# Optimization experiments

Hardware: AMD Instinct MI355X
Metric: run time of the kernel (lower is better)

## Reference

```python
import jax, jax.numpy as jnp
import numpy as np

B, CIN, X, Y = 4, 3, 128, 128
D, L, DEPTH, OUT = 64, 8, 4, 1
GRID_RANGE = 1.0
LN_EPS = 1e-5
YR = Y // 2 + 1


def _build_phi_f():
    # 1D Hilbert-matrix eigenbases along each axis, outer product, then rfft2.
    def top_eigvecs(n):
        i = np.arange(n)
        Z = 1.0 / (i[:, None] + i[None, :] + 1.0)  # Hilbert matrix, float64
        w, V = np.linalg.eigh(Z)
        idx = np.argsort(-w)[:L]
        return V.T[idx]  # (L, n)

    Vx = top_eigvecs(X)
    Vy = top_eigvecs(Y)
    phi = Vx[:, :, None] * Vy[:, None, :]  # (L, X, Y) separable eigenfunctions
    Phi_f = np.fft.rfft2(phi, s=(X, Y))  # (L, X, YR)
    return jnp.asarray(Phi_f, dtype=jnp.complex64)


def setup_inputs() -> dict:
    key = jax.random.key(0)
    ks = jax.random.split(key, 16)
    u = lambda k, shape, bound: jax.random.uniform(k, shape, jnp.float32, -bound, bound)
    inv = 1.0 / np.sqrt(D)
    inp = {
        "x": jax.random.normal(ks[0], (B, CIN, X, Y), jnp.float32),
        "Phi_f": _build_phi_f(),  # constant buffer
        "lift_w": u(ks[1], (D, CIN + 2), 1.0 / np.sqrt(CIN + 2)),
        "lift_b": u(ks[2], (D,), 1.0 / np.sqrt(CIN + 2)),
        "Theta": u(ks[3], (DEPTH, L, D, D), 1.0 / D),  # kaiming_uniform(a=sqrt(5)) ~ U(-1/d, 1/d)
        "glu_val_w": u(ks[4], (DEPTH, D, D), inv),
        "glu_val_b": u(ks[5], (DEPTH, D), inv),
        "glu_gate_w": u(ks[6], (DEPTH, D, D), inv),
        "glu_gate_b": u(ks[7], (DEPTH, D), inv),
        "ln_g": jnp.ones((DEPTH, D), jnp.float32),
        "ln_b": jnp.zeros((DEPTH, D), jnp.float32),
        "head_w": u(ks[8], (OUT, D), inv),
        "head_b": u(ks[9], (OUT,), inv),
    }
    return inp


def _stu_layer(h, Phi_f, Theta, vw, vb, gw, gb, g, b):
    # LayerNorm over channel dim (torch LayerNorm on channels-last view)
    ht = jnp.transpose(h, (0, 2, 3, 1))  # (B, X, Y, D)
    mu = jnp.mean(ht, axis=-1, keepdims=True)
    var = jnp.var(ht, axis=-1, keepdims=True)
    zt = (ht - mu) * jax.lax.rsqrt(var + LN_EPS) * g + b
    z = jnp.transpose(zt, (0, 3, 1, 2))  # (B, D, X, Y)

    Xf = jnp.fft.rfftn(z, axes=(-2, -1))  # (B, D, X, YR) complex
    Uf = Xf[:, :, None, :, :] * jnp.conj(Phi_f)[None, None]  # (B, D, L, X, YR)
    U = jnp.fft.irfftn(Uf, s=(X, Y), axes=(-2, -1))  # (B, D, L, X, Y)
    # einsum('bdlxy,lhd->bhlxy') followed by sum over l, fused:
    S = jnp.einsum("bdlxy,lhd->bhxy", U, Theta)

    V = jnp.einsum("bhxy,oh->boxy", S, vw) + vb[None, :, None, None]
    G = jax.nn.sigmoid(jnp.einsum("bhxy,oh->boxy", S, gw) + gb[None, :, None, None])
    return h + V * G


def reference(x, Phi_f, lift_w, lift_b, Theta, glu_val_w, glu_val_b,
              glu_gate_w, glu_gate_b, ln_g, ln_b, head_w, head_b):
    bsz = x.shape[0]
    # add_2d_grid: append yy, xx coordinate channels
    ys = jnp.linspace(0.0, GRID_RANGE, X, dtype=x.dtype)
    xs = jnp.linspace(0.0, GRID_RANGE, Y, dtype=x.dtype)
    yy, xx = jnp.meshgrid(ys, xs, indexing="ij")
    yy = jnp.broadcast_to(yy[None, None], (bsz, 1, X, Y))
    xx = jnp.broadcast_to(xx[None, None], (bsz, 1, X, Y))
    h = jnp.concatenate([x, yy, xx], axis=1)  # (B, CIN+2, X, Y)

    # LocalLift2D with kernel_size=1 -> pointwise conv
    h = jnp.einsum("bcxy,dc->bdxy", h, lift_w) + lift_b[None, :, None, None]

    for i in range(DEPTH):
        h = _stu_layer(h, Phi_f, Theta[i], glu_val_w[i], glu_val_b[i],
                       glu_gate_w[i], glu_gate_b[i], ln_g[i], ln_b[i])

    y = jnp.einsum("bdxy,od->boxy", h, head_w) + head_b[None, :, None, None]
    return y
```

## Files before the change

kernel.cpp:

```cpp
#include <hip/hip_runtime.h>
#include <math.h>
#include <string.h>


#define NXY 16384

#define OFF_V       16
#define OFF_MC      1040
#define OFF_THETAA  132112
#define OFF_AG      263184
#define OFF_Z       295952
#define OFF_H       4490256
#define OFF_P       8684560
#define WS_NEED_F   25461776ULL

typedef short short8 __attribute__((ext_vector_type(8)));
typedef float float4m __attribute__((ext_vector_type(4)));

__device__ __forceinline__ unsigned short bf_rn(float f) {
    unsigned u = __float_as_uint(f);
    u += 0x7fffu + ((u >> 16) & 1u);
    return (unsigned short)(u >> 16);
}
__device__ __forceinline__ float bf_tof(unsigned short s) {
    return __uint_as_float(((unsigned)s) << 16);
}

__global__ void poison_out(float* out) { out[0] = 1e9f; }


static float vhost[1024];

static void host_hilbert_topk(float* outv) {
    static double Vs[8][128];
    static double W[8][128];
    double recip[256];
    for (int i = 0; i < 256; i++) recip[i] = 1.0 / (double)(i + 1);
    for (int j = 0; j < 8; j++)
        for (int i = 0; i < 128; i++) Vs[j][i] = recip[i + j];
    for (int outer = 0; outer < 25; outer++) {
        for (int half = 0; half < 2; half++) {
            for (int j = 0; j < 8; j++)
                for (int i = 0; i < 128; i++) {
                    double s = 0.0;
                    for (int k = 0; k < 128; k++) s += Vs[j][k] * recip[i + k];
                    W[j][i] = s;
                }
            memcpy(Vs, W, sizeof(Vs));
        }
        for (int j = 0; j < 8; j++) {
            for (int p = 0; p < j; p++) {
                double d = 0.0;
                for (int i = 0; i < 128; i++) d += Vs[j][i] * Vs[p][i];
                for (int i = 0; i < 128; i++) Vs[j][i] -= d * Vs[p][i];
            }
            double nn = 0.0;
            for (int i = 0; i < 128; i++) nn += Vs[j][i] * Vs[j][i];
            double inv = 1.0 / sqrt(nn);
            for (int i = 0; i < 128; i++) Vs[j][i] *= inv;
        }
    }
    for (int j = 0; j < 8; j++)
        for (int i = 0; i < 128; i++) outv[j * 128 + i] = (float)Vs[j][i];
}

namespace {
struct VInit {
    VInit() { host_hilbert_topk(vhost); }
};
VInit vinit_once;
}

__global__ void build_mct(const float* __restrict__ v, unsigned short* __restrict__ McT) {
    int l = blockIdx.y;
    int idx = blockIdx.x * 256 + threadIdx.x;
    int r = idx >> 7, k = idx & 127;
    McT[l * 16384 + idx] = bf_rn(v[l * 128 + ((k - r) & 127)]);
}


__global__ void build_thetaAHL(const float* __restrict__ Theta, unsigned short* __restrict__ ThA) {
    int i = blockIdx.x * 256 + threadIdx.x;
    int k = i & 127; int r = i >> 7;
    int m = r & 127; r >>= 7;
    int tile = r & 3; int dep = r >> 2;
    int l2 = m >> 6, hch = m & 63, d = k & 63;
    float f = Theta[(((dep * 8 + tile * 2 + l2) * 64) + hch) * 64 + d];
    unsigned short hb = bf_rn(f);
    ThA[i] = (k < 64) ? hb : bf_rn(f - bf_tof(hb));
}

__global__ void build_AG(const float* __restrict__ vw, const float* __restrict__ gw,
                         float* __restrict__ AG) {
    int i = blockIdx.x * 256 + threadIdx.x;
    int m = i & 127; int r = i >> 7; int h = r & 63; int dep = r >> 6;
    int o = m >> 1;
    const float* W = (m & 1) ? gw : vw;
    AG[i] = W[(dep * 64 + o) * 64 + h];
}


__global__ void lift_ln(const float* __restrict__ x, const float* __restrict__ lw,
                        const float* __restrict__ lb, const float* __restrict__ g0,
                        const float* __restrict__ b0, float* __restrict__ h,
                        unsigned short* __restrict__ zT) {
    __shared__ float w[320];
    __shared__ float bsm[64];
    __shared__ float gs[64], bs[64];
    int tid = threadIdx.x;
    for (int i = tid; i < 320; i += 256) w[i] = lw[i];
    if (tid < 64) { bsm[tid] = lb[tid]; gs[tid] = g0[tid]; bs[tid] = b0[tid]; }
    __syncthreads();
    int b = blockIdx.y;
    int xy = blockIdx.x * 256 + tid;
    int xi = xy >> 7, yi = xy & 127;
    float c0 = x[(size_t)(b * 3 + 0) * NXY + xy];
    float c1 = x[(size_t)(b * 3 + 1) * NXY + xy];
    float c2 = x[(size_t)(b * 3 + 2) * NXY + xy];
    float yyv = xi * (1.0f / 127.0f), xxv = yi * (1.0f / 127.0f);
    float vv[64];
    float sum = 0.f;
#pragma unroll
    for (int d = 0; d < 64; d++) {
        float acc = bsm[d] + w[d * 5] * c0 + w[d * 5 + 1] * c1 + w[d * 5 + 2] * c2
                  + w[d * 5 + 3] * yyv + w[d * 5 + 4] * xxv;
        vv[d] = acc;
        sum += acc;
        h[(size_t)(b * 64 + d) * NXY + xy] = acc;
    }
    float mu = sum * (1.0f / 64.0f);
    float vs = 0.f;
#pragma unroll
    for (int d = 0; d < 64; d++) { float t = vv[d] - mu; vs += t * t; }
    float inv = rsqrtf(vs * (1.0f / 64.0f) + 1e-5f);
    unsigned short t16[64];
#pragma unroll
    for (int d = 0; d < 64; d++) t16[d] = bf_rn((vv[d] - mu) * inv * gs[d] + bs[d]);
    unsigned short* zp = zT + ((size_t)b * NXY + xy) * 64;
#pragma unroll
    for (int i = 0; i < 8; i++) {
        uint4 pk;
        pk.x = (unsigned)t16[8 * i + 0] | ((unsigned)t16[8 * i + 1] << 16);
        pk.y = (unsigned)t16[8 * i + 2] | ((unsigned)t16[8 * i + 3] << 16);
        pk.z = (unsigned)t16[8 * i + 4] | ((unsigned)t16[8 * i + 5] << 16);
        pk.w = (unsigned)t16[8 * i + 6] | ((unsigned)t16[8 * i + 7] << 16);
        *(uint4*)(zp + 8 * i) = pk;
    }
}

__global__ void head_kernel(const float* __restrict__ h, const float* __restrict__ hw,
                            const float* __restrict__ hb, float* __restrict__ out) {
    __shared__ float w[64];
    int tid = threadIdx.x;
    if (tid < 64) w[tid] = hw[tid];
    __syncthreads();
    int b = blockIdx.y;
    int xy = blockIdx.x * 256 + tid;
    float acc = hb[0];
    for (int d = 0; d < 64; d++) acc += h[(size_t)(b * 64 + d) * NXY + xy] * w[d];
    out[(size_t)b * NXY + xy] = acc;
}

__device__ __forceinline__ int sw_idx(int row, int k) {
    return row * 128 + ((((k >> 3) ^ (row & 7)) << 3) | (k & 7));
}


__launch_bounds__(256)
__global__ void k1_mfma(const unsigned short* __restrict__ zT,
                        const unsigned short* __restrict__ ThA,
                        unsigned short* __restrict__ P) {
    __shared__ unsigned short st[16384];
    const int lhtile = blockIdx.x, x = blockIdx.y, b = blockIdx.z;
    const int tid = threadIdx.x;
    const int wid = tid >> 6, lane = tid & 63;
    const int ln15 = lane & 15, q = lane >> 4;
    const int ko = q * 8;
    const unsigned short* Ab = ThA + lhtile * 16384;
    const unsigned short* Bb = zT + ((size_t)b * NXY + x * 128) * 64;

    float4m acc[2][8];
#pragma unroll
    for (int mt = 0; mt < 2; mt++)
#pragma unroll
        for (int nt = 0; nt < 8; nt++) acc[mt][nt] = (float4m){0.f, 0.f, 0.f, 0.f};

#pragma unroll
    for (int k0 = 0; k0 < 128; k0 += 32) {
        short8 a[2];
#pragma unroll
        for (int mt = 0; mt < 2; mt++)
            a[mt] = *(const short8*)(Ab + (wid * 32 + mt * 16 + ln15) * 128 + k0 + ko);
        int d0 = (k0 & 63) + ko;
#pragma unroll
        for (int nt = 0; nt < 8; nt++) {
            int n = nt * 16 + ln15;
            short8 bf = *(const short8*)(Bb + n * 64 + d0);
#pragma unroll
            for (int mt = 0; mt < 2; mt++)
                acc[mt][nt] = __builtin_amdgcn_mfma_f32_16x16x32_bf16(a[mt], bf, acc[mt][nt], 0, 0, 0);
        }
    }
#pragma unroll
    for (int mt = 0; mt < 2; mt++)
#pragma unroll
        for (int nt = 0; nt < 8; nt++) {
            int y = nt * 16 + ln15;
            int r0 = wid * 32 + mt * 16 + q * 4;
            float av[4] = {acc[mt][nt].x, acc[mt][nt].y, acc[mt][nt].z, acc[mt][nt].w};
#pragma unroll
            for (int r = 0; r < 4; r++) st[sw_idx(r0 + r, y)] = bf_rn(av[r]);
        }
    __syncthreads();
    unsigned short* Pb = P + (size_t)(b * 512 + lhtile * 128) * NXY + x * 128;
#pragma unroll
    for (int i = 0; i < 8; i++) {
        int idx = i * 256 + tid;
        int m = idx >> 4, c = idx & 15;
        *(uint4*)(Pb + (size_t)m * NXY + c * 8) = *(const uint4*)&st[sw_idx(m, c * 8)];
    }
}


__launch_bounds__(256)
__global__ void corr2q(unsigned short* __restrict__ P,
                       const unsigned short* __restrict__ McT) {
    __shared__ unsigned short Tt[16384];
    const int hh = blockIdx.x, l = blockIdx.y, b = blockIdx.z;
    unsigned short* plane = P + ((size_t)(b * 8 + l) * 64 + hh) * NXY;
    const unsigned short* Mc = McT + l * 16384;
    const int tid = threadIdx.x;
    const int wid = tid >> 6, lane = tid & 63;
    const int ln15 = lane & 15, q = lane >> 4;
    const int ko = q * 8;

    float4m acc[2][8];
#pragma unroll
    for (int mt = 0; mt < 2; mt++)
#pragma unroll
        for (int nt = 0; nt < 8; nt++) acc[mt][nt] = (float4m){0.f, 0.f, 0.f, 0.f};

#pragma unroll
    for (int k0 = 0; k0 < 128; k0 += 32) {
        short8 a[2];
#pragma unroll
        for (int mt = 0; mt < 2; mt++)
            a[mt] = *(const short8*)(plane + (wid * 32 + mt * 16 + ln15) * 128 + k0 + ko);
#pragma unroll
        for (int nt = 0; nt < 8; nt++) {
            int n = nt * 16 + ln15;
            short8 bf = *(const short8*)(Mc + n * 128 + k0 + ko);
#pragma unroll
            for (int mt = 0; mt < 2; mt++)
                acc[mt][nt] = __builtin_amdgcn_mfma_f32_16x16x32_bf16(a[mt], bf, acc[mt][nt], 0, 0, 0);
        }
    }
#pragma unroll
    for (int mt = 0; mt < 2; mt++)
#pragma unroll
        for (int nt = 0; nt < 8; nt++) {
            int yo = nt * 16 + ln15;
            int x0 = wid * 32 + mt * 16 + q * 4;
            float av[4] = {acc[mt][nt].x, acc[mt][nt].y, acc[mt][nt].z, acc[mt][nt].w};
            unsigned short hs[4];
#pragma unroll
            for (int r = 0; r < 4; r++) hs[r] = bf_rn(av[r]);
            uint2 pk;
            pk.x = (unsigned)hs[0] | ((unsigned)hs[1] << 16);
            pk.y = (unsigned)hs[2] | ((unsigned)hs[3] << 16);
            *(uint2*)&Tt[sw_idx(yo, x0)] = pk;
        }
    __syncthreads();

#pragma unroll
    for (int mt = 0; mt < 2; mt++)
#pragma unroll
        for (int nt = 0; nt < 8; nt++) acc[mt][nt] = (float4m){0.f, 0.f, 0.f, 0.f};
#pragma unroll
    for (int k0 = 0; k0 < 128; k0 += 32) {
        short8 a[2];
#pragma unroll
        for (int mt = 0; mt < 2; mt++)
            a[mt] = *(const short8*)(Mc + (wid * 32 + mt * 16 + ln15) * 128 + k0 + ko);
#pragma unroll
        for (int nt = 0; nt < 8; nt++) {
            int n = nt * 16 + ln15;
            short8 bf = *(const short8*)&Tt[sw_idx(n, k0 + ko)];
#pragma unroll
            for (int mt = 0; mt < 2; mt++)
                acc[mt][nt] = __builtin_amdgcn_mfma_f32_16x16x32_bf16(a[mt], bf, acc[mt][nt], 0, 0, 0);
        }
    }
    __syncthreads();
#pragma unroll
    for (int mt = 0; mt < 2; mt++)
#pragma unroll
        for (int nt = 0; nt < 8; nt++) {
            int y = nt * 16 + ln15;
            int x0 = wid * 32 + mt * 16 + q * 4;
            float av[4] = {acc[mt][nt].x, acc[mt][nt].y, acc[mt][nt].z, acc[mt][nt].w};
#pragma unroll
            for (int r = 0; r < 4; r++) Tt[sw_idx(x0 + r, y)] = bf_rn(av[r]);
        }
    __syncthreads();
#pragma unroll
    for (int i = 0; i < 8; i++) {
        int idx = i * 256 + tid;
        int xr = idx >> 4, c = idx & 15;
        *(uint4*)(plane + xr * 128 + c * 8) = *(const uint4*)&Tt[sw_idx(xr, c * 8)];
    }
}


template <int KTOT, long long BS1, long long PSTR, int NPART>
__launch_bounds__(256)
__global__ void glu_ln(const float* __restrict__ A0,
                       const unsigned short* __restrict__ B0, long long bsx, long long bsz,
                       float* __restrict__ C0, long long csx, long long csz, long long csm,
                       const float* __restrict__ e_vb, const float* __restrict__ e_gb,
                       const float* __restrict__ lngn, const float* __restrict__ lnbn,
                       unsigned short* __restrict__ zT) {
    constexpr int KS = 16;
    __shared__ float As[KS][132];
    __shared__ float Bs[KS][132];
    __shared__ float hn[64][129];
    const int tid = threadIdx.x;
    const int tm = tid >> 4, tn = tid & 15;
    const int m0 = tm * 8, n0 = tn * 8;
    const float* Ab = A0;
    const unsigned short* Bb = B0 + (long long)blockIdx.x * bsx + (long long)blockIdx.z * bsz;
    float* Cb = C0 + (long long)blockIdx.x * csx + (long long)blockIdx.z * csz;

    float acc[8][8];
#pragma unroll
    for (int i = 0; i < 8; i++)
#pragma unroll
        for (int j = 0; j < 8; j++) acc[i][j] = 0.f;

    for (int k0 = 0; k0 < KTOT; k0 += KS) {
#pragma unroll
        for (int i = 0; i < 2; i++) {
            int idx = tid + i * 256;
            int k = idx >> 5, f4 = (idx & 31) * 4;
            float4 v = *(const float4*)(Ab + (long long)(k0 + k) * 128 + f4);
            *(float4*)&As[k][f4] = v;
        }
#pragma unroll
        for (int i = 0; i < 2; i++) {
            int idx = tid + i * 256;
            int k = idx >> 5, f4 = (idx & 31) * 4;
            const unsigned short* bp = Bb + (long long)(k0 + k) * BS1 + f4;
            float vx = 0.f, vy = 0.f, vz = 0.f, vw = 0.f;
#pragma unroll
            for (int p = 0; p < NPART; p++) {
                uint2 t = *(const uint2*)(bp + (long long)p * PSTR);
                vx += bf_tof((unsigned short)(t.x & 0xffff));
                vy += bf_tof((unsigned short)(t.x >> 16));
                vz += bf_tof((unsigned short)(t.y & 0xffff));
                vw += bf_tof((unsigned short)(t.y >> 16));
            }
            Bs[k][f4] = vx; Bs[k][f4 + 1] = vy; Bs[k][f4 + 2] = vz; Bs[k][f4 + 3] = vw;
        }
        __syncthreads();
#pragma unroll
        for (int kk = 0; kk < KS; kk++) {
            float4 a0 = *(const float4*)&As[kk][m0];
            float4 a1 = *(const float4*)&As[kk][m0 + 4];
            float4 b0 = *(const float4*)&Bs[kk][n0];
            float4 b1 = *(const float4*)&Bs[kk][n0 + 4];
            float av[8] = {a0.x, a0.y, a0.z, a0.w, a1.x, a1.y, a1.z, a1.w};
            float bv[8] = {b0.x, b0.y, b0.z, b0.w, b1.x, b1.y, b1.z, b1.w};
#pragma unroll
            for (int i = 0; i < 8; i++)
#pragma unroll
                for (int j = 0; j < 8; j++) acc[i][j] += av[i] * bv[j];
        }
        __syncthreads();
    }

#pragma unroll
    for (int i = 0; i < 4; i++) {
        int o = (m0 >> 1) + i;
        float vbv = e_vb[o], gbv = e_gb[o];
        float* hp = Cb + (long long)o * csm + n0;
        float4 h0 = *(float4*)hp;
        float4 h1 = *(float4*)(hp + 4);
        float hv[8] = {h0.x, h0.y, h0.z, h0.w, h1.x, h1.y, h1.z, h1.w};
#pragma unroll
        for (int j = 0; j < 8; j++) {
            float V = acc[2 * i][j] + vbv;
            float G = acc[2 * i + 1][j] + gbv;
            float s = 1.0f / (1.0f + expf(-G));
            hv[j] += V * s;
            hn[o][n0 + j] = hv[j];
        }
        float4 o0 = {hv[0], hv[1], hv[2], hv[3]};
        float4 o1 = {hv[4], hv[5], hv[6], hv[7]};
        *(float4*)hp = o0;
        *(float4*)(hp + 4) = o1;
    }

    if (lngn != nullptr) {
        __syncthreads();
        if (tid < 128) {
            int xy = tid;
            float sum = 0.f;
#pragma unroll
            for (int d = 0; d < 64; d++) sum += hn[d][xy];
            float mu = sum * (1.0f / 64.0f);
            float vs = 0.f;
#pragma unroll
            for (int d = 0; d < 64; d++) { float t = hn[d][xy] - mu; vs += t * t; }
            float inv = rsqrtf(vs * (1.0f / 64.0f) + 1e-5f);
            unsigned short t16[64];
#pragma unroll
            for (int d = 0; d < 64; d++)
                t16[d] = bf_rn((hn[d][xy] - mu) * inv * lngn[d] + lnbn[d]);
            unsigned short* zp = zT + ((size_t)blockIdx.z * NXY + blockIdx.x * 128 + xy) * 64;
#pragma unroll
            for (int i = 0; i < 8; i++) {
                uint4 pk;
                pk.x = (unsigned)t16[8 * i + 0] | ((unsigned)t16[8 * i + 1] << 16);
                pk.y = (unsigned)t16[8 * i + 2] | ((unsigned)t16[8 * i + 3] << 16);
                pk.z = (unsigned)t16[8 * i + 4] | ((unsigned)t16[8 * i + 5] << 16);
                pk.w = (unsigned)t16[8 * i + 6] | ((unsigned)t16[8 * i + 7] << 16);
                *(uint4*)(zp + 8 * i) = pk;
            }
        }
    }
}


extern "C" void kernel_launch(void* const* d_in, const int* in_sizes, int n_in,
                              void* d_out, int out_size, void* d_ws, size_t ws_size,
                              hipStream_t stream) {
    const float* x      = (const float*)d_in[0];
    const float* lift_w = (const float*)d_in[2];
    const float* lift_b = (const float*)d_in[3];
    const float* Theta  = (const float*)d_in[4];
    const float* vw     = (const float*)d_in[5];
    const float* vb     = (const float*)d_in[6];
    const float* gw     = (const float*)d_in[7];
    const float* gb     = (const float*)d_in[8];
    const float* ln_g   = (const float*)d_in[9];
    const float* ln_b   = (const float*)d_in[10];
    const float* head_w = (const float*)d_in[11];
    const float* head_b = (const float*)d_in[12];
    float* out = (float*)d_out;
    float* ws = (float*)d_ws;
    (void)in_sizes; (void)n_in; (void)out_size;

    float* v      = ws + OFF_V;
    unsigned short* McT = (unsigned short*)(ws + OFF_MC);
    unsigned short* ThA = (unsigned short*)(ws + OFF_THETAA);
    float* AG     = ws + OFF_AG;
    unsigned short* zT = (unsigned short*)(ws + OFF_Z);
    float* h      = ws + OFF_H;
    unsigned short* P = (unsigned short*)(ws + OFF_P);

    hipMemcpyAsync(v, vhost, sizeof(vhost), hipMemcpyHostToDevice, stream);

    build_mct<<<dim3(64, 8), 256, 0, stream>>>(v, McT);
    build_thetaAHL<<<1024, 256, 0, stream>>>(Theta, ThA);
    build_AG<<<128, 256, 0, stream>>>(vw, gw, AG);

    lift_ln<<<dim3(64, 4), 256, 0, stream>>>(x, lift_w, lift_b, ln_g, ln_b, h, zT);

    for (int dep = 0; dep < 4; dep++) {
        k1_mfma<<<dim3(4, 128, 4), 256, 0, stream>>>(zT, ThA + dep * 65536, P);

        corr2q<<<dim3(64, 8, 4), 256, 0, stream>>>(P, McT);

        const float* lngn = (dep < 3) ? (ln_g + (dep + 1) * 64) : nullptr;
        const float* lnbn = (dep < 3) ? (ln_b + (dep + 1) * 64) : nullptr;
        glu_ln<64, 16384LL, 1048576LL, 8><<<dim3(128, 1, 4), 256, 0, stream>>>(
            AG + dep * 8192,
            P, 128, 8388608,
            h, 128, 1048576, 16384,
            vb + dep * 64, gb + dep * 64,
            lngn, lnbn, zT);
    }

    head_kernel<<<dim3(64, 4), 256, 0, stream>>>(h, head_w, head_b, out);

    if (ws_size < WS_NEED_F * 4ULL) {
        poison_out<<<1, 1, 0, stream>>>(out);
    }
}
```

Before: 591.7 us.

## Fuse head projection into last GLU kernel and widen corr2q to 512 threads

The separate head kernel is removed. The last layer's glu_ln now computes the output projection from its shared-memory tile and skips writing h back to global memory. Separately, corr2q moves from 4 to 8 waves per block, each handling one 16-row M tile instead of two. This halves per-thread accumulators and adds latency hiding, at the cost of reloading the B fragments per wave.

```diff
diff --git a/kernel.cpp b/kernel.cpp
--- a/kernel.cpp
+++ b/kernel.cpp
@@ -148,19 +148,6 @@
     }
 }
 
-__global__ void head_kernel(const float* __restrict__ h, const float* __restrict__ hw,
-                            const float* __restrict__ hb, float* __restrict__ out) {
-    __shared__ float w[64];
-    int tid = threadIdx.x;
-    if (tid < 64) w[tid] = hw[tid];
-    __syncthreads();
-    int b = blockIdx.y;
-    int xy = blockIdx.x * 256 + tid;
-    float acc = hb[0];
-    for (int d = 0; d < 64; d++) acc += h[(size_t)(b * 64 + d) * NXY + xy] * w[d];
-    out[(size_t)b * NXY + xy] = acc;
-}
-
 __device__ __forceinline__ int sw_idx(int row, int k) {
     return row * 128 + ((((k >> 3) ^ (row & 7)) << 3) | (k & 7));
 }
@@ -222,7 +209,7 @@
 }
 
 
-__launch_bounds__(256)
+__launch_bounds__(512)
 __global__ void corr2q(unsigned short* __restrict__ P,
                        const unsigned short* __restrict__ McT) {
     __shared__ unsigned short Tt[16384];
@@ -233,79 +220,61 @@
     const int wid = tid >> 6, lane = tid & 63;
     const int ln15 = lane & 15, q = lane >> 4;
     const int ko = q * 8;
-
-    float4m acc[2][8];
-#pragma unroll
-    for (int mt = 0; mt < 2; mt++)
-#pragma unroll
-        for (int nt = 0; nt < 8; nt++) acc[mt][nt] = (float4m){0.f, 0.f, 0.f, 0.f};
+    const int m = wid * 16 + ln15;
+    const int x0 = wid * 16 + q * 4;
+
+    float4m acc[8];
+#pragma unroll
+    for (int nt = 0; nt < 8; nt++) acc[nt] = (float4m){0.f, 0.f, 0.f, 0.f};
 
 #pragma unroll
     for (int k0 = 0; k0 < 128; k0 += 32) {
-        short8 a[2];
-#pragma unroll
-        for (int mt = 0; mt < 2; mt++)
-            a[mt] = *(const short8*)(plane + (wid * 32 + mt * 16 + ln15) * 128 + k0 + ko);
+        short8 a = *(const short8*)(plane + m * 128 + k0 + ko);
 #pragma unroll
         for (int nt = 0; nt < 8; nt++) {
             int n = nt * 16 + ln15;
             short8 bf = *(const short8*)(Mc + n * 128 + k0 + ko);
-#pragma unroll
-            for (int mt = 0; mt < 2; mt++)
-                acc[mt][nt] = __builtin_amdgcn_mfma_f32_16x16x32_bf16(a[mt], bf, acc[mt][nt], 0, 0, 0);
-        }
-    }
-#pragma unroll
-    for (int mt = 0; mt < 2; mt++)
-#pragma unroll
-        for (int nt = 0; nt < 8; nt++) {
-            int yo = nt * 16 + ln15;
-            int x0 = wid * 32 + mt * 16 + q * 4;
-            float av[4] = {acc[mt][nt].x, acc[mt][nt].y, acc[mt][nt].z, acc[mt][nt].w};
-            unsigned short hs[4];
-#pragma unroll
-            for (int r = 0; r < 4; r++) hs[r] = bf_rn(av[r]);
-            uint2 pk;
-            pk.x = (unsigned)hs[0] | ((unsigned)hs[1] << 16);
-            pk.y = (unsigned)hs[2] | ((unsigned)hs[3] << 16);
-            *(uint2*)&Tt[sw_idx(yo, x0)] = pk;
-        }
+            acc[nt] = __builtin_amdgcn_mfma_f32_16x16x32_bf16(a, bf, acc[nt], 0, 0, 0);
+        }
+    }
+#pragma unroll
+    for (int nt = 0; nt < 8; nt++) {
+        int yo = nt * 16 + ln15;
+        float av[4] = {acc[nt].x, acc[nt].y, acc[nt].z, acc[nt].w};
+        unsigned short hs[4];
+#pragma unroll
+        for (int r = 0; r < 4; r++) hs[r] = bf_rn(av[r]);
+        uint2 pk;
+        pk.x = (unsigned)hs[0] | ((unsigned)hs[1] << 16);
+        pk.y = (unsigned)hs[2] | ((unsigned)hs[3] << 16);
+        *(uint2*)&Tt[sw_idx(yo, x0)] = pk;
+    }
     __syncthreads();
 
 #pragma unroll
-    for (int mt = 0; mt < 2; mt++)
-#pragma unroll
-        for (int nt = 0; nt < 8; nt++) acc[mt][nt] = (float4m){0.f, 0.f, 0.f, 0.f};
+    for (int nt = 0; nt < 8; nt++) acc[nt] = (float4m){0.f, 0.f, 0.f, 0.f};
 #pragma unroll
     for (int k0 = 0; k0 < 128; k0 += 32) {
-        short8 a[2];
-#pragma unroll
-        for (int mt = 0; mt < 2; mt++)
-            a[mt] = *(const short8*)(Mc + (wid * 32 + mt * 16 + ln15) * 128 + k0 + ko);
+        short8 a = *(const short8*)(Mc + m * 128 + k0 + ko);
 #pragma unroll
         for (int nt = 0; nt < 8; nt++) {
             int n = nt * 16 + ln15;
             short8 bf = *(const short8*)&Tt[sw_idx(n, k0 + ko)];
-#pragma unroll
-            for (int mt = 0; mt < 2; mt++)
-                acc[mt][nt] = __builtin_amdgcn_mfma_f32_16x16x32_bf16(a[mt], bf, acc[mt][nt], 0, 0, 0);
+            acc[nt] = __builtin_amdgcn_mfma_f32_16x16x32_bf16(a, bf, acc[nt], 0, 0, 0);
         }
     }
     __syncthreads();
 #pragma unroll
-    for (int mt = 0; mt < 2; mt++)
-#pragma unroll
-        for (int nt = 0; nt < 8; nt++) {
-            int y = nt * 16 + ln15;
-            int x0 = wid * 32 + mt * 16 + q * 4;
-            float av[4] = {acc[mt][nt].x, acc[mt][nt].y, acc[mt][nt].z, acc[mt][nt].w};
-#pragma unroll
-            for (int r = 0; r < 4; r++) Tt[sw_idx(x0 + r, y)] = bf_rn(av[r]);
-        }
+    for (int nt = 0; nt < 8; nt++) {
+        int y = nt * 16 + ln15;
+        float av[4] = {acc[nt].x, acc[nt].y, acc[nt].z, acc[nt].w};
+#pragma unroll
+        for (int r = 0; r < 4; r++) Tt[sw_idx(x0 + r, y)] = bf_rn(av[r]);
+    }
     __syncthreads();
 #pragma unroll
-    for (int i = 0; i < 8; i++) {
-        int idx = i * 256 + tid;
+    for (int i = 0; i < 4; i++) {
+        int idx = i * 512 + tid;
         int xr = idx >> 4, c = idx & 15;
         *(uint4*)(plane + xr * 128 + c * 8) = *(const uint4*)&Tt[sw_idx(xr, c * 8)];
     }
@@ -319,7 +288,9 @@
                        float* __restrict__ C0, long long csx, long long csz, long long csm,
                        const float* __restrict__ e_vb, const float* __restrict__ e_gb,
                        const float* __restrict__ lngn, const float* __restrict__ lnbn,
-                       unsigned short* __restrict__ zT) {
+                       unsigned short* __restrict__ zT,
+                       const float* __restrict__ hw, const float* __restrict__ hbp,
+                       float* __restrict__ outp) {
     constexpr int KS = 16;
     __shared__ float As[KS][132];
     __shared__ float Bs[KS][132];
@@ -394,10 +365,12 @@
             hv[j] += V * s;
             hn[o][n0 + j] = hv[j];
         }
-        float4 o0 = {hv[0], hv[1], hv[2], hv[3]};
-        float4 o1 = {hv[4], hv[5], hv[6], hv[7]};
-        *(float4*)hp = o0;
-        *(float4*)(hp + 4) = o1;
+        if (outp == nullptr) {
+            float4 o0 = {hv[0], hv[1], hv[2], hv[3]};
+            float4 o1 = {hv[4], hv[5], hv[6], hv[7]};
+            *(float4*)hp = o0;
+            *(float4*)(hp + 4) = o1;
+        }
     }
 
     if (lngn != nullptr) {
@@ -426,6 +399,15 @@
                 pk.w = (unsigned)t16[8 * i + 6] | ((unsigned)t16[8 * i + 7] << 16);
                 *(uint4*)(zp + 8 * i) = pk;
             }
+        }
+    } else if (outp != nullptr) {
+        __syncthreads();
+        if (tid < 128) {
+            int xy = tid;
+            float acch = hbp[0];
+#pragma unroll
+            for (int d = 0; d < 64; d++) acch += hn[d][xy] * hw[d];
+            outp[(size_t)blockIdx.z * NXY + blockIdx.x * 128 + xy] = acch;
         }
     }
 }
@@ -469,19 +451,19 @@
     for (int dep = 0; dep < 4; dep++) {
         k1_mfma<<<dim3(4, 128, 4), 256, 0, stream>>>(zT, ThA + dep * 65536, P);
 
-        corr2q<<<dim3(64, 8, 4), 256, 0, stream>>>(P, McT);
+        corr2q<<<dim3(64, 8, 4), 512, 0, stream>>>(P, McT);
 
         const float* lngn = (dep < 3) ? (ln_g + (dep + 1) * 64) : nullptr;
         const float* lnbn = (dep < 3) ? (ln_b + (dep + 1) * 64) : nullptr;
+        float* outp = (dep == 3) ? out : nullptr;
         glu_ln<64, 16384LL, 1048576LL, 8><<<dim3(128, 1, 4), 256, 0, stream>>>(
             AG + dep * 8192,
             P, 128, 8388608,
             h, 128, 1048576, 16384,
             vb + dep * 64, gb + dep * 64,
-            lngn, lnbn, zT);
-    }
-
-    head_kernel<<<dim3(64, 4), 256, 0, stream>>>(h, head_w, head_b, out);
+            lngn, lnbn, zT,
+            head_w, head_b, outp);
+    }
 
     if (ws_size < WS_NEED_F * 4ULL) {
         poison_out<<<1, 1, 0, stream>>>(out);
```

Result: slower. 673.4 us (+13.8%).
